# Optimization experiments

Hardware: AMD Instinct MI355X
Metric: run time of the kernel (lower is better)

Reference implementation:

```python
import jax, jax.numpy as jnp
import numpy as np

NUM_GRAPHS = 100  # batch of graphs for pooling (dgl.max_nodes / WeightAndSum)


def _glorot(k, shape):
    lim = np.sqrt(6.0 / (shape[0] + shape[1])).astype(np.float32)
    return jax.random.uniform(k, shape, jnp.float32, -lim, lim)


def setup_inputs() -> dict:
    key = jax.random.key(0)
    ks = jax.random.split(key, 10)
    N, E, D, H = 100000, 1600000, 128, 128
    node_feats = jax.random.normal(ks[0], (N, D), dtype=jnp.float32)
    src = jax.random.randint(ks[1], (E,), 0, N, dtype=jnp.int32)
    dst = jax.random.randint(ks[2], (E,), 0, N, dtype=jnp.int32)
    graph_ids = jnp.sort(jax.random.randint(ks[3], (N,), 0, NUM_GRAPHS, dtype=jnp.int32))
    W1 = _glorot(ks[4], (D, H)); b1 = jnp.zeros((H,), jnp.float32)
    W2 = _glorot(ks[5], (H, H)); b2 = jnp.zeros((H,), jnp.float32)
    W3 = _glorot(ks[6], (H, H)); b3 = jnp.zeros((H,), jnp.float32)
    W_pool = _glorot(ks[7], (H, 1)); b_pool = jnp.zeros((1,), jnp.float32)
    return {"node_feats": node_feats, "src": src, "dst": dst, "graph_ids": graph_ids,
            "W1": W1, "b1": b1, "W2": W2, "b2": b2, "W3": W3, "b3": b3,
            "W_pool": W_pool, "b_pool": b_pool}


def _gcn_layer(h, W, b, src, dst, norm_src, norm_dst, N):
    # DGL GraphConv, norm='both': D_dst^{-1/2} (A^T (D_src^{-1/2} X W)) + b
    h = (h * norm_src[:, None]) @ W                      # [N, H]
    agg = jax.ops.segment_sum(h[src], dst, num_segments=N)  # gather + scatter-add
    return agg * norm_dst[:, None] + b


def reference(node_feats, src, dst, graph_ids, W1, b1, W2, b2, W3, b3, W_pool, b_pool):
    N = node_feats.shape[0]
    # dgl.add_self_loop (allow_zero_in_degree=False)
    loops = jnp.arange(N, dtype=src.dtype)
    src_sl = jnp.concatenate([src, loops])
    dst_sl = jnp.concatenate([dst, loops])
    ones = jnp.ones(src_sl.shape, jnp.float32)
    out_deg = jax.ops.segment_sum(ones, src_sl, num_segments=N)
    in_deg = jax.ops.segment_sum(ones, dst_sl, num_segments=N)
    norm_src = jax.lax.rsqrt(jnp.maximum(out_deg, 1.0))
    norm_dst = jax.lax.rsqrt(jnp.maximum(in_deg, 1.0))
    h = node_feats
    for W, b in ((W1, b1), (W2, b2), (W3, b3)):
        h = jax.nn.relu(_gcn_layer(h, W, b, src_sl, dst_sl, norm_src, norm_dst, N))
    # pooling_func: WeightAndSum (sigmoid-gated weighted sum per graph) + max_nodes
    w = jax.nn.sigmoid(h @ W_pool + b_pool)              # [N, 1]
    g_sum = jax.ops.segment_sum(h * w, graph_ids, num_segments=NUM_GRAPHS)
    g_max = jax.ops.segment_max(h, graph_ids, num_segments=NUM_GRAPHS)
    return jnp.concatenate([g_sum, g_max], axis=1)       # [G, 2H]
```

## Files before the change

kernel.cpp:

```cpp
#include <hip/hip_runtime.h>
#include <hip/hip_bf16.h>

#define DIM 128
#define CAP 64
#define NBMAX 64
#define BCAP 36864
#define CSPLIT 8

typedef __attribute__((ext_vector_type(8))) short bf16x8;
typedef __attribute__((ext_vector_type(4))) float f32x4;
union U16 { uint4 u; bf16x8 b; };

__device__ __forceinline__ unsigned short f2bf(float f) {
    unsigned u = __float_as_uint(f);
    unsigned r = (u + 0x7fffu + ((u >> 16) & 1u)) >> 16;
    return (unsigned short)r;
}
__device__ __forceinline__ unsigned pack2bf(float a, float b) {
    return (unsigned)f2bf(a) | ((unsigned)f2bf(b) << 16);
}
__device__ __forceinline__ float2 unpack2bf(unsigned v) {
    float2 r;
    r.x = __uint_as_float(v << 16);
    r.y = __uint_as_float(v & 0xffff0000u);
    return r;
}
__device__ __forceinline__ void accum8s(float* acc, uint4 v, float s) {
    float2 f0 = unpack2bf(v.x), f1 = unpack2bf(v.y);
    float2 f2 = unpack2bf(v.z), f3 = unpack2bf(v.w);
    acc[0] += s * f0.x; acc[1] += s * f0.y; acc[2] += s * f1.x; acc[3] += s * f1.y;
    acc[4] += s * f2.x; acc[5] += s * f2.y; acc[6] += s * f3.x; acc[7] += s * f3.y;
}

__global__ __launch_bounds__(256) void k_bin(const int* __restrict__ src,
                                             const int* __restrict__ dst, int E,
                                             unsigned* __restrict__ binD,
                                             unsigned short* __restrict__ binS,
                                             int* __restrict__ cntD,
                                             int* __restrict__ cntS, int NB, int binGrid,
                                             const float* __restrict__ W1,
                                             const float* __restrict__ W2,
                                             const float* __restrict__ W3,
                                             unsigned* __restrict__ wT1g,
                                             unsigned* __restrict__ wT2g,
                                             unsigned* __restrict__ wT3g) {
    __shared__ int hD[NBMAX], hS[NBMAX], bD[NBMAX], bS[NBMAX];
    int t = threadIdx.x;
    if ((int)blockIdx.x >= binGrid) {
        int w = blockIdx.x - binGrid;
        const float* Wsrc = (w == 0) ? W1 : (w == 1) ? W2 : W3;
        unsigned* wTg = (w == 0) ? wT1g : (w == 1) ? wT2g : wT3g;
        int n = t >> 1;
        int kp0 = (t & 1) * 32;
#pragma unroll
        for (int i = 0; i < 32; i++) {
            int kp = kp0 + i;
            wTg[n * 64 + kp] = pack2bf(Wsrc[(2 * kp) * DIM + n], Wsrc[(2 * kp + 1) * DIM + n]);
        }
        return;
    }
    if (t < NB) { hD[t] = 0; hS[t] = 0; }
    __syncthreads();
    int e0 = blockIdx.x * 1024 + t * 4;
    int s[4], d[4];
    bool v[4];
#pragma unroll
    for (int i = 0; i < 4; i++) {
        v[i] = (e0 + i) < E;
        s[i] = 0; d[i] = 0;
        if (v[i]) { s[i] = src[e0 + i]; d[i] = dst[e0 + i]; }
    }
#pragma unroll
    for (int i = 0; i < 4; i++) {
        if (v[i]) {
            atomicAdd(&hD[d[i] >> 11], 1);
            atomicAdd(&hS[s[i] >> 11], 1);
        }
    }
    __syncthreads();
    if (t < NB) {
        bD[t] = atomicAdd(&cntD[t], hD[t]);
        bS[t] = atomicAdd(&cntS[t], hS[t]);
        hD[t] = 0; hS[t] = 0;
    }
    __syncthreads();
#pragma unroll
    for (int i = 0; i < 4; i++) {
        if (v[i]) {
            int bd = d[i] >> 11;
            int r = atomicAdd(&hD[bd], 1);
            int idx = bD[bd] + r;
            if (idx < BCAP)
                binD[bd * BCAP + idx] = ((unsigned)(d[i] & 2047) << 17) | (unsigned)s[i];
            int bs = s[i] >> 11;
            int r2 = atomicAdd(&hS[bs], 1);
            int idx2 = bS[bs] + r2;
            if (idx2 < BCAP) binS[bs * BCAP + idx2] = (unsigned short)(s[i] & 2047);
        }
    }
}

__global__ __launch_bounds__(256) void k_mega(const unsigned* __restrict__ binD,
                                              const unsigned short* __restrict__ binS,
                                              const int* __restrict__ cntD,
                                              const int* __restrict__ cntS,
                                              int* __restrict__ in_cnt,
                                              int* __restrict__ out_cnt,
                                              int* __restrict__ csr_pad,
                                              const float* __restrict__ x,
                                              const unsigned* __restrict__ wT1g,
                                              unsigned* __restrict__ xwb, int N,
                                              int NB) {
    __shared__ __align__(16) char smem[34816];
    int bid = blockIdx.x;
    int t = threadIdx.x;

    if (bid < NB * CSPLIT) {
        int b = bid / CSPLIT;
        int sub = bid - b * CSPLIT;
        int* h = (int*)smem;
        int* bArr = ((int*)smem) + 2048;
        for (int j = t; j < 2048; j += 256) h[j] = 0;
        __syncthreads();
        int base = b << 11;
        int nE = cntD[b];
        if (nE > BCAP) nE = BCAP;
        int chunk = (nE + CSPLIT - 1) / CSPLIT;
        int i0 = sub * chunk;
        int i1 = i0 + chunk;
        if (i1 > nE) i1 = nE;
        const unsigned* bb = &binD[b * BCAP];
        for (int i = i0 + t * 4; i < i1; i += 1024) {
            unsigned e[4];
            int k = i1 - i;
            if (k > 4) k = 4;
#pragma unroll
            for (int j = 0; j < 4; j++)
                if (j < k) e[j] = bb[i + j];
#pragma unroll
            for (int j = 0; j < 4; j++)
                if (j < k) atomicAdd(&h[e[j] >> 17], 1);
        }
        __syncthreads();
        for (int j = t; j < 2048; j += 256) {
            int hv = h[j];
            bArr[j] = hv ? atomicAdd(&in_cnt[base + j], hv) : 0;
            h[j] = 0;
        }
        __syncthreads();
        for (int i = i0 + t * 4; i < i1; i += 1024) {
            unsigned e[4];
            int k = i1 - i;
            if (k > 4) k = 4;
#pragma unroll
            for (int j = 0; j < 4; j++)
                if (j < k) e[j] = bb[i + j];
#pragma unroll
            for (int j = 0; j < 4; j++)
                if (j < k) {
                    int dl = (int)(e[j] >> 17);
                    int pos = bArr[dl] + atomicAdd(&h[dl], 1);
                    if (pos < CAP)
                        csr_pad[(size_t)(base + dl) * CAP + pos] = (int)(e[j] & 0x1FFFFu);
                }
        }
        return;
    }
    if (bid < 2 * NB * CSPLIT) {
        int bb2 = bid - NB * CSPLIT;
        int b = bb2 / CSPLIT;
        int sub = bb2 - b * CSPLIT;
        int* hist = (int*)smem;
        for (int j = t; j < 2048; j += 256) hist[j] = 0;
        __syncthreads();
        int base = b << 11;
        int nE = cntS[b];
        if (nE > BCAP) nE = BCAP;
        int chunk = (nE + CSPLIT - 1) / CSPLIT;
        int i0 = sub * chunk;
        int i1 = i0 + chunk;
        if (i1 > nE) i1 = nE;
        const unsigned short* bs = &binS[b * BCAP];
        for (int i = i0 + t * 4; i < i1; i += 1024) {
            unsigned short e[4];
            int k = i1 - i;
            if (k > 4) k = 4;
#pragma unroll
            for (int j = 0; j < 4; j++)
                if (j < k) e[j] = bs[i + j];
#pragma unroll
            for (int j = 0; j < 4; j++)
                if (j < k) atomicAdd(&hist[(int)e[j]], 1);
        }
        __syncthreads();
        for (int j = t; j < 2048; j += 256) {
            int hv = hist[j];
            if (hv) atomicAdd(&out_cnt[base + j], hv);
        }
        return;
    }
    int gb = bid - 2 * NB * CSPLIT;
    unsigned* wT = (unsigned*)smem;
#pragma unroll
    for (int i = 0; i < 8; i++) {
        int idx = t + i * 256;
        int row = idx >> 4;
        int col = idx & 15;
        *(uint4*)&wT[row * 68 + col * 4] = ((const uint4*)wT1g)[idx];
    }
    __syncthreads();
    int wave = t >> 6, lane = t & 63;
    int quad = lane >> 4, c = lane & 15;
    int m = gb * 64 + wave * 16 + c;
    bool mv = m < N;
    f32x4 acc[8];
#pragma unroll
    for (int i = 0; i < 8; i++) acc[i] = (f32x4){0.f, 0.f, 0.f, 0.f};

#pragma unroll
    for (int ks = 0; ks < 4; ks++) {
        U16 av;
        if (mv) {
            const float4* xr = (const float4*)&x[(size_t)m * DIM + ks * 32 + quad * 8];
            float4 f0 = xr[0], f1 = xr[1];
            av.u.x = pack2bf(f0.x, f0.y);
            av.u.y = pack2bf(f0.z, f0.w);
            av.u.z = pack2bf(f1.x, f1.y);
            av.u.w = pack2bf(f1.z, f1.w);
        } else {
            av.u = make_uint4(0, 0, 0, 0);
        }
#pragma unroll
        for (int cb = 0; cb < 8; cb++) {
            U16 bv;
            bv.u = *(const uint4*)&wT[(cb * 16 + c) * 68 + ks * 16 + quad * 4];
            acc[cb] = __builtin_amdgcn_mfma_f32_16x16x32_bf16(av.b, bv.b, acc[cb], 0, 0, 0);
        }
    }
    int rowBase = gb * 64 + wave * 16 + quad * 4;
#pragma unroll
    for (int r = 0; r < 4; r++) {
        int rowN = rowBase + r;
#pragma unroll
        for (int cb = 0; cb < 8; cb++) {
            float v = acc[cb][r];
            float vn = __shfl_xor(v, 1, 64);
            if (((c & 1) == 0) && rowN < N)
                xwb[rowN * 64 + cb * 8 + (c >> 1)] = pack2bf(v, vn);
        }
    }
}

__global__ __launch_bounds__(256) void k_agg1(const uint4* __restrict__ xwb4,
                                              const int* __restrict__ in_cnt,
                                              const int* __restrict__ out_cnt,
                                              const int* __restrict__ csr_pad,
                                              const float* __restrict__ bias,
                                              uint4* __restrict__ hb4, int N) {
    int gid = blockIdx.x * blockDim.x + threadIdx.x;
    int n = gid >> 6;
    int lane = gid & 63;
    if (n >= N) return;
    int quad = lane >> 4;
    int c = lane & 15;

    float acc[8];
#pragma unroll
    for (int i = 0; i < 8; i++) acc[i] = 0.f;

    if (quad == 0) {
        float sn = rsqrtf((float)(out_cnt[n] + 1));
        accum8s(acc, xwb4[n * 16 + c], sn);
    }
    int deg_true = in_cnt[n];
    int deg = deg_true > CAP ? CAP : deg_true;
    const int* row = &csr_pad[(size_t)n * CAP];
    int p = 0;
    for (; p + 16 <= deg; p += 16) {
        int s0 = row[p + quad];
        int s1 = row[p + 4 + quad];
        int s2 = row[p + 8 + quad];
        int s3 = row[p + 12 + quad];
        uint4 v0 = xwb4[s0 * 16 + c];
        uint4 v1 = xwb4[s1 * 16 + c];
        uint4 v2 = xwb4[s2 * 16 + c];
        uint4 v3 = xwb4[s3 * 16 + c];
        float n0 = rsqrtf((float)(out_cnt[s0] + 1));
        float n1 = rsqrtf((float)(out_cnt[s1] + 1));
        float n2 = rsqrtf((float)(out_cnt[s2] + 1));
        float n3 = rsqrtf((float)(out_cnt[s3] + 1));
        accum8s(acc, v0, n0);
        accum8s(acc, v1, n1);
        accum8s(acc, v2, n2);
        accum8s(acc, v3, n3);
    }
    for (; p + 8 <= deg; p += 8) {
        int s0 = row[p + quad];
        int s1 = row[p + 4 + quad];
        uint4 v0 = xwb4[s0 * 16 + c];
        uint4 v1 = xwb4[s1 * 16 + c];
        float n0 = rsqrtf((float)(out_cnt[s0] + 1));
        float n1 = rsqrtf((float)(out_cnt[s1] + 1));
        accum8s(acc, v0, n0);
        accum8s(acc, v1, n1);
    }
    for (; p < deg; p += 4) {
        int pe = p + quad;
        int s = row[pe < deg ? pe : p];
        uint4 v = xwb4[s * 16 + c];
        float ns = rsqrtf((float)(out_cnt[s] + 1));
        if (pe < deg) accum8s(acc, v, ns);
    }
#pragma unroll
    for (int i = 0; i < 8; i++) {
        acc[i] += __shfl_xor(acc[i], 16, 64);
        acc[i] += __shfl_xor(acc[i], 32, 64);
    }
    float ndv = rsqrtf((float)(deg_true + 1));
    if (quad == 0) {
        float4 b0 = ((const float4*)bias)[2 * c];
        float4 b1 = ((const float4*)bias)[2 * c + 1];
        uint4 w;
        w.x = pack2bf(fmaxf(acc[0] * ndv + b0.x, 0.f), fmaxf(acc[1] * ndv + b0.y, 0.f));
        w.y = pack2bf(fmaxf(acc[2] * ndv + b0.z, 0.f), fmaxf(acc[3] * ndv + b0.w, 0.f));
        w.z = pack2bf(fmaxf(acc[4] * ndv + b1.x, 0.f), fmaxf(acc[5] * ndv + b1.y, 0.f));
        w.w = pack2bf(fmaxf(acc[6] * ndv + b1.z, 0.f), fmaxf(acc[7] * ndv + b1.w, 0.f));
        hb4[n * 16 + c] = w;
    }
}

__global__ __launch_bounds__(256) void k_xw_mfma(const unsigned* __restrict__ hb,
                                                 const int* __restrict__ out_cnt,
                                                 const unsigned* __restrict__ wTg,
                                                 unsigned* __restrict__ xwb, int N) {
    __shared__ unsigned wT[128 * 68];
    int t = threadIdx.x;
#pragma unroll
    for (int i = 0; i < 8; i++) {
        int idx = t + i * 256;
        int row = idx >> 4;
        int col = idx & 15;
        *(uint4*)&wT[row * 68 + col * 4] = ((const uint4*)wTg)[idx];
    }
    __syncthreads();
    int wave = t >> 6, lane = t & 63;
    int quad = lane >> 4, c = lane & 15;
    int m = blockIdx.x * 64 + wave * 16 + c;
    bool mv = m < N;
    f32x4 acc[8];
#pragma unroll
    for (int i = 0; i < 8; i++) acc[i] = (f32x4){0.f, 0.f, 0.f, 0.f};

#pragma unroll
    for (int ks = 0; ks < 4; ks++) {
        U16 av;
        if (mv) av.u = *(const uint4*)&hb[m * 64 + ks * 16 + quad * 4];
        else av.u = make_uint4(0, 0, 0, 0);
#pragma unroll
        for (int cb = 0; cb < 8; cb++) {
            U16 bv;
            bv.u = *(const uint4*)&wT[(cb * 16 + c) * 68 + ks * 16 + quad * 4];
            acc[cb] = __builtin_amdgcn_mfma_f32_16x16x32_bf16(av.b, bv.b, acc[cb], 0, 0, 0);
        }
    }
    int rowBase = blockIdx.x * 64 + wave * 16 + quad * 4;
#pragma unroll
    for (int r = 0; r < 4; r++) {
        int rowN = rowBase + r;
        float nrm = (rowN < N) ? rsqrtf((float)(out_cnt[rowN] + 1)) : 0.f;
#pragma unroll
        for (int cb = 0; cb < 8; cb++) {
            float v = acc[cb][r] * nrm;
            float vn = __shfl_xor(v, 1, 64);
            if (((c & 1) == 0) && rowN < N)
                xwb[rowN * 64 + cb * 8 + (c >> 1)] = pack2bf(v, vn);
        }
    }
}

template <bool GATED>
__device__ __forceinline__ void agg_body(const uint4* __restrict__ xwb4,
                                         const int* __restrict__ in_cnt,
                                         const int* __restrict__ csr_pad,
                                         const float* __restrict__ bias,
                                         uint4* __restrict__ hb4,
                                         const float* __restrict__ Wp,
                                         const float* __restrict__ bp,
                                         float* __restrict__ wg, int N) {
    int gid = blockIdx.x * blockDim.x + threadIdx.x;
    int n = gid >> 6;
    int lane = gid & 63;
    if (n >= N) return;
    int quad = lane >> 4;
    int c = lane & 15;

    float acc[8];
#pragma unroll
    for (int i = 0; i < 8; i++) acc[i] = 0.f;

    if (quad == 0) {
        accum8s(acc, xwb4[n * 16 + c], 1.f);
    }
    int deg_true = in_cnt[n];
    int deg = deg_true > CAP ? CAP : deg_true;
    const int* row = &csr_pad[(size_t)n * CAP];
    int p = 0;
    for (; p + 16 <= deg; p += 16) {
        int s0 = row[p + quad];
        int s1 = row[p + 4 + quad];
        int s2 = row[p + 8 + quad];
        int s3 = row[p + 12 + quad];
        uint4 v0 = xwb4[s0 * 16 + c];
        uint4 v1 = xwb4[s1 * 16 + c];
        uint4 v2 = xwb4[s2 * 16 + c];
        uint4 v3 = xwb4[s3 * 16 + c];
        accum8s(acc, v0, 1.f);
        accum8s(acc, v1, 1.f);
        accum8s(acc, v2, 1.f);
        accum8s(acc, v3, 1.f);
    }
    for (; p + 8 <= deg; p += 8) {
        int s0 = row[p + quad];
        int s1 = row[p + 4 + quad];
        uint4 v0 = xwb4[s0 * 16 + c];
        uint4 v1 = xwb4[s1 * 16 + c];
        accum8s(acc, v0, 1.f);
        accum8s(acc, v1, 1.f);
    }
    for (; p < deg; p += 4) {
        int pe = p + quad;
        int s = row[pe < deg ? pe : p];
        uint4 v = xwb4[s * 16 + c];
        if (pe < deg) accum8s(acc, v, 1.f);
    }
#pragma unroll
    for (int i = 0; i < 8; i++) {
        acc[i] += __shfl_xor(acc[i], 16, 64);
        acc[i] += __shfl_xor(acc[i], 32, 64);
    }
    float ndv = rsqrtf((float)(deg_true + 1));
    float4 b0 = ((const float4*)bias)[2 * c];
    float4 b1 = ((const float4*)bias)[2 * c + 1];
    float o[8];
    o[0] = fmaxf(acc[0] * ndv + b0.x, 0.f);
    o[1] = fmaxf(acc[1] * ndv + b0.y, 0.f);
    o[2] = fmaxf(acc[2] * ndv + b0.z, 0.f);
    o[3] = fmaxf(acc[3] * ndv + b0.w, 0.f);
    o[4] = fmaxf(acc[4] * ndv + b1.x, 0.f);
    o[5] = fmaxf(acc[5] * ndv + b1.y, 0.f);
    o[6] = fmaxf(acc[6] * ndv + b1.z, 0.f);
    o[7] = fmaxf(acc[7] * ndv + b1.w, 0.f);
    if (quad == 0) {
        uint4 w;
        w.x = pack2bf(o[0], o[1]);
        w.y = pack2bf(o[2], o[3]);
        w.z = pack2bf(o[4], o[5]);
        w.w = pack2bf(o[6], o[7]);
        hb4[n * 16 + c] = w;
    }
    if (GATED) {
        float s = 0.f;
        if (quad == 0) {
            float4 w0 = ((const float4*)Wp)[2 * c];
            float4 w1 = ((const float4*)Wp)[2 * c + 1];
            s = o[0] * w0.x + o[1] * w0.y + o[2] * w0.z + o[3] * w0.w +
                o[4] * w1.x + o[5] * w1.y + o[6] * w1.z + o[7] * w1.w;
        }
        s += __shfl_xor(s, 1, 64);
        s += __shfl_xor(s, 2, 64);
        s += __shfl_xor(s, 4, 64);
        s += __shfl_xor(s, 8, 64);
        if (lane == 0) wg[n] = 1.f / (1.f + expf(-(s + bp[0])));
    }
}

__global__ __launch_bounds__(256) void k_agg(const uint4* __restrict__ xwb4,
                                             const int* __restrict__ in_cnt,
                                             const int* __restrict__ csr_pad,
                                             const float* __restrict__ bias,
                                             uint4* __restrict__ hb4, int N) {
    agg_body<false>(xwb4, in_cnt, csr_pad, bias, hb4, nullptr, nullptr, nullptr, N);
}

__global__ __launch_bounds__(256) void k_agg_gate(const uint4* __restrict__ xwb4,
                                                  const int* __restrict__ in_cnt,
                                                  const int* __restrict__ csr_pad,
                                                  const float* __restrict__ bias,
                                                  uint4* __restrict__ hb4,
                                                  const float* __restrict__ Wp,
                                                  const float* __restrict__ bp,
                                                  float* __restrict__ wg, int N) {
    agg_body<true>(xwb4, in_cnt, csr_pad, bias, hb4, Wp, bp, wg, N);
}

__device__ __forceinline__ int lower_bound(const int* a, int n, int key) {
    int lo = 0, hi = n;
    while (lo < hi) {
        int m = (lo + hi) >> 1;
        if (a[m] < key) lo = m + 1;
        else hi = m;
    }
    return lo;
}

__global__ __launch_bounds__(64) void k_pool(const unsigned* __restrict__ hb,
                                             const float* __restrict__ wg,
                                             const int* __restrict__ gids,
                                             float* __restrict__ out, int N) {
    int g = blockIdx.x >> 4;
    int part = blockIdx.x & 15;
    int t = threadIdx.x;
    int start = lower_bound(gids, N, g);
    int end = lower_bound(gids, N, g + 1);
    float2 sum = {0.f, 0.f}, mx = {0.f, 0.f};
    for (int n = start + part; n < end; n += 16) {
        float w = wg[n];
        float2 v = unpack2bf(hb[n * 64 + t]);
        sum.x += v.x * w;
        sum.y += v.y * w;
        mx.x = fmaxf(mx.x, v.x);
        mx.y = fmaxf(mx.y, v.y);
    }
    atomicAdd(&out[g * 256 + 2 * t], sum.x);
    atomicAdd(&out[g * 256 + 2 * t + 1], sum.y);
    atomicMax((int*)&out[g * 256 + 128 + 2 * t], __float_as_int(mx.x));
    atomicMax((int*)&out[g * 256 + 128 + 2 * t + 1], __float_as_int(mx.y));
}

extern "C" void kernel_launch(void* const* d_in, const int* in_sizes, int n_in,
                              void* d_out, int out_size, void* d_ws, size_t ws_size,
                              hipStream_t stream) {
    const float* node_feats = (const float*)d_in[0];
    const int* src = (const int*)d_in[1];
    const int* dst = (const int*)d_in[2];
    const int* gids = (const int*)d_in[3];
    const float* W1 = (const float*)d_in[4];
    const float* b1 = (const float*)d_in[5];
    const float* W2 = (const float*)d_in[6];
    const float* b2 = (const float*)d_in[7];
    const float* W3 = (const float*)d_in[8];
    const float* b3 = (const float*)d_in[9];
    const float* Wp = (const float*)d_in[10];
    const float* bp = (const float*)d_in[11];
    float* out = (float*)d_out;

    const int N = in_sizes[3];
    const int E = in_sizes[1];
    const int G = out_size / 256;
    const int NB = (N + 2047) >> 11;

    char* ws = (char*)d_ws;
    size_t o = 0;
    int* cntD = (int*)(ws + o);          o += NBMAX * 4;
    int* cntS = (int*)(ws + o);          o += NBMAX * 4;
    int* in_cnt = (int*)(ws + o);        o += (size_t)N * 4;
    int* out_cnt = (int*)(ws + o);       o += (size_t)N * 4;
    size_t zero_bytes = o;
    float* wg = (float*)(ws + o);        o += (size_t)N * 4;
    o = (o + 15) & ~15ull;
    unsigned* wT1g = (unsigned*)(ws + o); o += 8192 * 4;
    unsigned* wT2g = (unsigned*)(ws + o); o += 8192 * 4;
    unsigned* wT3g = (unsigned*)(ws + o); o += 8192 * 4;
    unsigned* binD = (unsigned*)(ws + o); o += (size_t)NBMAX * BCAP * 4;
    unsigned short* binS = (unsigned short*)(ws + o); o += (size_t)NBMAX * BCAP * 2;
    o = (o + 15) & ~15ull;
    int* csr_pad = (int*)(ws + o);       o += (size_t)N * CAP * 4;
    unsigned* xwb = (unsigned*)(ws + o); o += (size_t)N * 64 * 4;
    unsigned* hb = (unsigned*)(ws + o);  o += (size_t)N * 64 * 4;
    (void)ws_size;

    (void)hipMemsetAsync(d_ws, 0, zero_bytes, stream);
    (void)hipMemsetAsync(d_out, 0, (size_t)out_size * 4, stream);

    int binGrid = (E + 1023) / 1024;
    int mmGrid = (N + 63) / 64;
    int aggGrid = ((N * 64) + 255) / 256;

    k_bin<<<binGrid + 3, 256, 0, stream>>>(src, dst, E, binD, binS, cntD, cntS, NB, binGrid,
                                           W1, W2, W3, wT1g, wT2g, wT3g);
    k_mega<<<2 * NB * CSPLIT + mmGrid, 256, 0, stream>>>(binD, binS, cntD, cntS, in_cnt,
                                                         out_cnt, csr_pad, node_feats,
                                                         wT1g, xwb, N, NB);
    k_agg1<<<aggGrid, 256, 0, stream>>>((const uint4*)xwb, in_cnt, out_cnt, csr_pad, b1,
                                        (uint4*)hb, N);
    k_xw_mfma<<<mmGrid, 256, 0, stream>>>(hb, out_cnt, wT2g, xwb, N);
    k_agg<<<aggGrid, 256, 0, stream>>>((const uint4*)xwb, in_cnt, csr_pad, b2,
                                       (uint4*)hb, N);
    k_xw_mfma<<<mmGrid, 256, 0, stream>>>(hb, out_cnt, wT3g, xwb, N);
    k_agg_gate<<<aggGrid, 256, 0, stream>>>((const uint4*)xwb, in_cnt, csr_pad, b3,
                                            (uint4*)hb, Wp, bp, wg, N);
    k_pool<<<G * 16, 64, 0, stream>>>(hb, wg, gids, out, N);
}
```

Baseline: 454.4 us.

## Map four nodes per wave in aggregation kernels and precompute source norms

The aggregation kernels now give each 16-lane group of a wave its own destination node and walk that node's edges serially, four at a time. Previously the four quads split one node's edges and then merged results with cross-quad shuffles. This removes the shuffle reduction, lets every lane do useful epilogue work and store, and launches a quarter as many threads. A new small kernel precomputes the per-node source-norm rsqrt once, so layer 1 no longer recomputes it for every edge, and accumulation uses fma with native bf16 conversion. The risk is divergence between the four nodes of a wave when their degrees differ, and slightly different memory-level parallelism per node.

```diff
diff --git a/kernel.cpp b/kernel.cpp
--- a/kernel.cpp
+++ b/kernel.cpp
@@ -9,7 +9,9 @@
 
 typedef __attribute__((ext_vector_type(8))) short bf16x8;
 typedef __attribute__((ext_vector_type(4))) float f32x4;
+typedef __bf16 bf16x2 __attribute__((ext_vector_type(2)));
 union U16 { uint4 u; bf16x8 b; };
+union UB { unsigned u; bf16x2 h; };
 
 __device__ __forceinline__ unsigned short f2bf(float f) {
     unsigned u = __float_as_uint(f);
@@ -30,6 +32,18 @@
     float2 f2 = unpack2bf(v.z), f3 = unpack2bf(v.w);
     acc[0] += s * f0.x; acc[1] += s * f0.y; acc[2] += s * f1.x; acc[3] += s * f1.y;
     acc[4] += s * f2.x; acc[5] += s * f2.y; acc[6] += s * f3.x; acc[7] += s * f3.y;
+}
+__device__ __forceinline__ void accum8m(float* acc, uint4 v, float s) {
+    UB w0, w1, w2, w3;
+    w0.u = v.x; w1.u = v.y; w2.u = v.z; w3.u = v.w;
+    acc[0] = fmaf((float)w0.h[0], s, acc[0]);
+    acc[1] = fmaf((float)w0.h[1], s, acc[1]);
+    acc[2] = fmaf((float)w1.h[0], s, acc[2]);
+    acc[3] = fmaf((float)w1.h[1], s, acc[3]);
+    acc[4] = fmaf((float)w2.h[0], s, acc[4]);
+    acc[5] = fmaf((float)w2.h[1], s, acc[5]);
+    acc[6] = fmaf((float)w3.h[0], s, acc[6]);
+    acc[7] = fmaf((float)w3.h[1], s, acc[7]);
 }
 
 __global__ __launch_bounds__(256) void k_bin(const int* __restrict__ src,
@@ -251,227 +265,109 @@
     }
 }
 
-__global__ __launch_bounds__(256) void k_agg1(const uint4* __restrict__ xwb4,
-                                              const int* __restrict__ in_cnt,
-                                              const int* __restrict__ out_cnt,
-                                              const int* __restrict__ csr_pad,
-                                              const float* __restrict__ bias,
-                                              uint4* __restrict__ hb4, int N) {
-    int gid = blockIdx.x * blockDim.x + threadIdx.x;
-    int n = gid >> 6;
-    int lane = gid & 63;
-    if (n >= N) return;
-    int quad = lane >> 4;
-    int c = lane & 15;
-
-    float acc[8];
-#pragma unroll
-    for (int i = 0; i < 8; i++) acc[i] = 0.f;
-
-    if (quad == 0) {
-        float sn = rsqrtf((float)(out_cnt[n] + 1));
-        accum8s(acc, xwb4[n * 16 + c], sn);
-    }
-    int deg_true = in_cnt[n];
-    int deg = deg_true > CAP ? CAP : deg_true;
-    const int* row = &csr_pad[(size_t)n * CAP];
-    int p = 0;
-    for (; p + 16 <= deg; p += 16) {
-        int s0 = row[p + quad];
-        int s1 = row[p + 4 + quad];
-        int s2 = row[p + 8 + quad];
-        int s3 = row[p + 12 + quad];
-        uint4 v0 = xwb4[s0 * 16 + c];
-        uint4 v1 = xwb4[s1 * 16 + c];
-        uint4 v2 = xwb4[s2 * 16 + c];
-        uint4 v3 = xwb4[s3 * 16 + c];
-        float n0 = rsqrtf((float)(out_cnt[s0] + 1));
-        float n1 = rsqrtf((float)(out_cnt[s1] + 1));
-        float n2 = rsqrtf((float)(out_cnt[s2] + 1));
-        float n3 = rsqrtf((float)(out_cnt[s3] + 1));
-        accum8s(acc, v0, n0);
-        accum8s(acc, v1, n1);
-        accum8s(acc, v2, n2);
-        accum8s(acc, v3, n3);
-    }
-    for (; p + 8 <= deg; p += 8) {
-        int s0 = row[p + quad];
-        int s1 = row[p + 4 + quad];
-        uint4 v0 = xwb4[s0 * 16 + c];
-        uint4 v1 = xwb4[s1 * 16 + c];
-        float n0 = rsqrtf((float)(out_cnt[s0] + 1));
-        float n1 = rsqrtf((float)(out_cnt[s1] + 1));
-        accum8s(acc, v0, n0);
-        accum8s(acc, v1, n1);
-    }
-    for (; p < deg; p += 4) {
-        int pe = p + quad;
-        int s = row[pe < deg ? pe : p];
-        uint4 v = xwb4[s * 16 + c];
-        float ns = rsqrtf((float)(out_cnt[s] + 1));
-        if (pe < deg) accum8s(acc, v, ns);
-    }
-#pragma unroll
-    for (int i = 0; i < 8; i++) {
-        acc[i] += __shfl_xor(acc[i], 16, 64);
-        acc[i] += __shfl_xor(acc[i], 32, 64);
-    }
-    float ndv = rsqrtf((float)(deg_true + 1));
-    if (quad == 0) {
-        float4 b0 = ((const float4*)bias)[2 * c];
-        float4 b1 = ((const float4*)bias)[2 * c + 1];
-        uint4 w;
-        w.x = pack2bf(fmaxf(acc[0] * ndv + b0.x, 0.f), fmaxf(acc[1] * ndv + b0.y, 0.f));
-        w.y = pack2bf(fmaxf(acc[2] * ndv + b0.z, 0.f), fmaxf(acc[3] * ndv + b0.w, 0.f));
-        w.z = pack2bf(fmaxf(acc[4] * ndv + b1.x, 0.f), fmaxf(acc[5] * ndv + b1.y, 0.f));
-        w.w = pack2bf(fmaxf(acc[6] * ndv + b1.z, 0.f), fmaxf(acc[7] * ndv + b1.w, 0.f));
-        hb4[n * 16 + c] = w;
-    }
-}
-
-__global__ __launch_bounds__(256) void k_xw_mfma(const unsigned* __restrict__ hb,
-                                                 const int* __restrict__ out_cnt,
-                                                 const unsigned* __restrict__ wTg,
-                                                 unsigned* __restrict__ xwb, int N) {
-    __shared__ unsigned wT[128 * 68];
-    int t = threadIdx.x;
-#pragma unroll
-    for (int i = 0; i < 8; i++) {
-        int idx = t + i * 256;
-        int row = idx >> 4;
-        int col = idx & 15;
-        *(uint4*)&wT[row * 68 + col * 4] = ((const uint4*)wTg)[idx];
-    }
-    __syncthreads();
-    int wave = t >> 6, lane = t & 63;
-    int quad = lane >> 4, c = lane & 15;
-    int m = blockIdx.x * 64 + wave * 16 + c;
-    bool mv = m < N;
-    f32x4 acc[8];
-#pragma unroll
-    for (int i = 0; i < 8; i++) acc[i] = (f32x4){0.f, 0.f, 0.f, 0.f};
-
-#pragma unroll
-    for (int ks = 0; ks < 4; ks++) {
-        U16 av;
-        if (mv) av.u = *(const uint4*)&hb[m * 64 + ks * 16 + quad * 4];
-        else av.u = make_uint4(0, 0, 0, 0);
-#pragma unroll
-        for (int cb = 0; cb < 8; cb++) {
-            U16 bv;
-            bv.u = *(const uint4*)&wT[(cb * 16 + c) * 68 + ks * 16 + quad * 4];
-            acc[cb] = __builtin_amdgcn_mfma_f32_16x16x32_bf16(av.b, bv.b, acc[cb], 0, 0, 0);
-        }
-    }
-    int rowBase = blockIdx.x * 64 + wave * 16 + quad * 4;
-#pragma unroll
-    for (int r = 0; r < 4; r++) {
-        int rowN = rowBase + r;
-        float nrm = (rowN < N) ? rsqrtf((float)(out_cnt[rowN] + 1)) : 0.f;
-#pragma unroll
-        for (int cb = 0; cb < 8; cb++) {
-            float v = acc[cb][r] * nrm;
-            float vn = __shfl_xor(v, 1, 64);
-            if (((c & 1) == 0) && rowN < N)
-                xwb[rowN * 64 + cb * 8 + (c >> 1)] = pack2bf(v, vn);
-        }
-    }
-}
-
-template <bool GATED>
+__global__ __launch_bounds__(256) void k_nrm(const int* __restrict__ out_cnt,
+                                             float* __restrict__ nsv, int N) {
+    int i = (blockIdx.x * 256 + threadIdx.x) * 4;
+    if (i + 3 < N) {
+        int4 d = *(const int4*)&out_cnt[i];
+        float4 r;
+        r.x = rsqrtf((float)(d.x + 1));
+        r.y = rsqrtf((float)(d.y + 1));
+        r.z = rsqrtf((float)(d.z + 1));
+        r.w = rsqrtf((float)(d.w + 1));
+        *(float4*)&nsv[i] = r;
+    } else {
+        for (int j = i; j < N && j < i + 4; j++) nsv[j] = rsqrtf((float)(out_cnt[j] + 1));
+    }
+}
+
+template <int MODE>
 __device__ __forceinline__ void agg_body(const uint4* __restrict__ xwb4,
                                          const int* __restrict__ in_cnt,
                                          const int* __restrict__ csr_pad,
+                                         const float* __restrict__ nsv,
                                          const float* __restrict__ bias,
                                          uint4* __restrict__ hb4,
                                          const float* __restrict__ Wp,
                                          const float* __restrict__ bp,
                                          float* __restrict__ wg, int N) {
-    int gid = blockIdx.x * blockDim.x + threadIdx.x;
-    int n = gid >> 6;
-    int lane = gid & 63;
-    if (n >= N) return;
-    int quad = lane >> 4;
-    int c = lane & 15;
+    int wid = (blockIdx.x * 256 + threadIdx.x) >> 6;
+    int lane = threadIdx.x & 63;
+    int g = lane >> 4, c = lane & 15;
+    int n = wid * 4 + g;
+    bool nv = n < N;
+    int deg_true = nv ? in_cnt[n] : 0;
+    int deg = deg_true > CAP ? CAP : deg_true;
+    float ndv = rsqrtf((float)(deg_true + 1));
+    const int* row = csr_pad + (size_t)n * CAP;
 
     float acc[8];
 #pragma unroll
     for (int i = 0; i < 8; i++) acc[i] = 0.f;
 
-    if (quad == 0) {
-        accum8s(acc, xwb4[n * 16 + c], 1.f);
-    }
-    int deg_true = in_cnt[n];
-    int deg = deg_true > CAP ? CAP : deg_true;
-    const int* row = &csr_pad[(size_t)n * CAP];
-    int p = 0;
-    for (; p + 16 <= deg; p += 16) {
-        int s0 = row[p + quad];
-        int s1 = row[p + 4 + quad];
-        int s2 = row[p + 8 + quad];
-        int s3 = row[p + 12 + quad];
-        uint4 v0 = xwb4[s0 * 16 + c];
-        uint4 v1 = xwb4[s1 * 16 + c];
-        uint4 v2 = xwb4[s2 * 16 + c];
-        uint4 v3 = xwb4[s3 * 16 + c];
-        accum8s(acc, v0, 1.f);
-        accum8s(acc, v1, 1.f);
-        accum8s(acc, v2, 1.f);
-        accum8s(acc, v3, 1.f);
-    }
-    for (; p + 8 <= deg; p += 8) {
-        int s0 = row[p + quad];
-        int s1 = row[p + 4 + quad];
-        uint4 v0 = xwb4[s0 * 16 + c];
-        uint4 v1 = xwb4[s1 * 16 + c];
-        accum8s(acc, v0, 1.f);
-        accum8s(acc, v1, 1.f);
-    }
-    for (; p < deg; p += 4) {
-        int pe = p + quad;
-        int s = row[pe < deg ? pe : p];
-        uint4 v = xwb4[s * 16 + c];
-        if (pe < deg) accum8s(acc, v, 1.f);
-    }
-#pragma unroll
-    for (int i = 0; i < 8; i++) {
-        acc[i] += __shfl_xor(acc[i], 16, 64);
-        acc[i] += __shfl_xor(acc[i], 32, 64);
-    }
-    float ndv = rsqrtf((float)(deg_true + 1));
+    if (nv) {
+        float s0 = (MODE == 0) ? nsv[n] : ndv;
+        accum8m(acc, xwb4[(size_t)n * 16 + c], s0);
+    }
+    for (int p = 0; p < deg; p += 4) {
+        int sidx[4];
+        uint4 gv[4];
+        float sc[4];
+        bool pv[4];
+#pragma unroll
+        for (int u = 0; u < 4; u++) {
+            pv[u] = (p + u) < deg;
+            sidx[u] = pv[u] ? row[p + u] : row[p];
+        }
+#pragma unroll
+        for (int u = 0; u < 4; u++) gv[u] = xwb4[(size_t)sidx[u] * 16 + c];
+#pragma unroll
+        for (int u = 0; u < 4; u++) sc[u] = (MODE == 0) ? nsv[sidx[u]] : ndv;
+#pragma unroll
+        for (int u = 0; u < 4; u++)
+            if (pv[u]) accum8m(acc, gv[u], sc[u]);
+    }
+
+    float mul = (MODE == 0) ? ndv : 1.f;
     float4 b0 = ((const float4*)bias)[2 * c];
     float4 b1 = ((const float4*)bias)[2 * c + 1];
     float o[8];
-    o[0] = fmaxf(acc[0] * ndv + b0.x, 0.f);
-    o[1] = fmaxf(acc[1] * ndv + b0.y, 0.f);
-    o[2] = fmaxf(acc[2] * ndv + b0.z, 0.f);
-    o[3] = fmaxf(acc[3] * ndv + b0.w, 0.f);
-    o[4] = fmaxf(acc[4] * ndv + b1.x, 0.f);
-    o[5] = fmaxf(acc[5] * ndv + b1.y, 0.f);
-    o[6] = fmaxf(acc[6] * ndv + b1.z, 0.f);
-    o[7] = fmaxf(acc[7] * ndv + b1.w, 0.f);
-    if (quad == 0) {
+    o[0] = fmaxf(acc[0] * mul + b0.x, 0.f);
+    o[1] = fmaxf(acc[1] * mul + b0.y, 0.f);
+    o[2] = fmaxf(acc[2] * mul + b0.z, 0.f);
+    o[3] = fmaxf(acc[3] * mul + b0.w, 0.f);
+    o[4] = fmaxf(acc[4] * mul + b1.x, 0.f);
+    o[5] = fmaxf(acc[5] * mul + b1.y, 0.f);
+    o[6] = fmaxf(acc[6] * mul + b1.z, 0.f);
+    o[7] = fmaxf(acc[7] * mul + b1.w, 0.f);
+    if (nv) {
         uint4 w;
         w.x = pack2bf(o[0], o[1]);
         w.y = pack2bf(o[2], o[3]);
         w.z = pack2bf(o[4], o[5]);
         w.w = pack2bf(o[6], o[7]);
-        hb4[n * 16 + c] = w;
-    }
-    if (GATED) {
-        float s = 0.f;
-        if (quad == 0) {
-            float4 w0 = ((const float4*)Wp)[2 * c];
-            float4 w1 = ((const float4*)Wp)[2 * c + 1];
-            s = o[0] * w0.x + o[1] * w0.y + o[2] * w0.z + o[3] * w0.w +
-                o[4] * w1.x + o[5] * w1.y + o[6] * w1.z + o[7] * w1.w;
-        }
+        hb4[(size_t)n * 16 + c] = w;
+    }
+    if (MODE == 2) {
+        float4 w0 = ((const float4*)Wp)[2 * c];
+        float4 w1 = ((const float4*)Wp)[2 * c + 1];
+        float s = o[0] * w0.x + o[1] * w0.y + o[2] * w0.z + o[3] * w0.w +
+                  o[4] * w1.x + o[5] * w1.y + o[6] * w1.z + o[7] * w1.w;
         s += __shfl_xor(s, 1, 64);
         s += __shfl_xor(s, 2, 64);
         s += __shfl_xor(s, 4, 64);
         s += __shfl_xor(s, 8, 64);
-        if (lane == 0) wg[n] = 1.f / (1.f + expf(-(s + bp[0])));
-    }
+        if (nv && c == 0) wg[n] = 1.f / (1.f + expf(-(s + bp[0])));
+    }
+}
+
+__global__ __launch_bounds__(256) void k_agg1(const uint4* __restrict__ xwb4,
+                                              const int* __restrict__ in_cnt,
+                                              const int* __restrict__ csr_pad,
+                                              const float* __restrict__ nsv,
+                                              const float* __restrict__ bias,
+                                              uint4* __restrict__ hb4, int N) {
+    agg_body<0>(xwb4, in_cnt, csr_pad, nsv, bias, hb4, nullptr, nullptr, nullptr, N);
 }
 
 __global__ __launch_bounds__(256) void k_agg(const uint4* __restrict__ xwb4,
@@ -479,7 +375,7 @@
                                              const int* __restrict__ csr_pad,
                                              const float* __restrict__ bias,
                                              uint4* __restrict__ hb4, int N) {
-    agg_body<false>(xwb4, in_cnt, csr_pad, bias, hb4, nullptr, nullptr, nullptr, N);
+    agg_body<1>(xwb4, in_cnt, csr_pad, nullptr, bias, hb4, nullptr, nullptr, nullptr, N);
 }
 
 __global__ __launch_bounds__(256) void k_agg_gate(const uint4* __restrict__ xwb4,
@@ -490,7 +386,56 @@
                                                   const float* __restrict__ Wp,
                                                   const float* __restrict__ bp,
                                                   float* __restrict__ wg, int N) {
-    agg_body<true>(xwb4, in_cnt, csr_pad, bias, hb4, Wp, bp, wg, N);
+    agg_body<2>(xwb4, in_cnt, csr_pad, nullptr, bias, hb4, Wp, bp, wg, N);
+}
+
+__global__ __launch_bounds__(256) void k_xw_mfma(const unsigned* __restrict__ hb,
+                                                 const int* __restrict__ out_cnt,
+                                                 const unsigned* __restrict__ wTg,
+                                                 unsigned* __restrict__ xwb, int N) {
+    __shared__ unsigned wT[128 * 68];
+    int t = threadIdx.x;
+#pragma unroll
+    for (int i = 0; i < 8; i++) {
+        int idx = t + i * 256;
+        int row = idx >> 4;
+        int col = idx & 15;
+        *(uint4*)&wT[row * 68 + col * 4] = ((const uint4*)wTg)[idx];
+    }
+    __syncthreads();
+    int wave = t >> 6, lane = t & 63;
+    int quad = lane >> 4, c = lane & 15;
+    int m = blockIdx.x * 64 + wave * 16 + c;
+    bool mv = m < N;
+    f32x4 acc[8];
+#pragma unroll
+    for (int i = 0; i < 8; i++) acc[i] = (f32x4){0.f, 0.f, 0.f, 0.f};
+
+#pragma unroll
+    for (int ks = 0; ks < 4; ks++) {
+        U16 av;
+        if (mv) av.u = *(const uint4*)&hb[m * 64 + ks * 16 + quad * 4];
+        else av.u = make_uint4(0, 0, 0, 0);
+#pragma unroll
+        for (int cb = 0; cb < 8; cb++) {
+            U16 bv;
+            bv.u = *(const uint4*)&wT[(cb * 16 + c) * 68 + ks * 16 + quad * 4];
+            acc[cb] = __builtin_amdgcn_mfma_f32_16x16x32_bf16(av.b, bv.b, acc[cb], 0, 0, 0);
+        }
+    }
+    int rowBase = blockIdx.x * 64 + wave * 16 + quad * 4;
+#pragma unroll
+    for (int r = 0; r < 4; r++) {
+        int rowN = rowBase + r;
+        float nrm = (rowN < N) ? rsqrtf((float)(out_cnt[rowN] + 1)) : 0.f;
+#pragma unroll
+        for (int cb = 0; cb < 8; cb++) {
+            float v = acc[cb][r] * nrm;
+            float vn = __shfl_xor(v, 1, 64);
+            if (((c & 1) == 0) && rowN < N)
+                xwb[rowN * 64 + cb * 8 + (c >> 1)] = pack2bf(v, vn);
+        }
+    }
 }
 
 __device__ __forceinline__ int lower_bound(const int* a, int n, int key) {
@@ -557,6 +502,7 @@
     int* out_cnt = (int*)(ws + o);       o += (size_t)N * 4;
     size_t zero_bytes = o;
     float* wg = (float*)(ws + o);        o += (size_t)N * 4;
+    float* nsv = (float*)(ws + o);       o += (size_t)N * 4;
     o = (o + 15) & ~15ull;
     unsigned* wT1g = (unsigned*)(ws + o); o += 8192 * 4;
     unsigned* wT2g = (unsigned*)(ws + o); o += 8192 * 4;
@@ -574,14 +520,16 @@
 
     int binGrid = (E + 1023) / 1024;
     int mmGrid = (N + 63) / 64;
-    int aggGrid = ((N * 64) + 255) / 256;
+    int aggGrid = (N + 15) / 16;
+    int nrmGrid = (N + 1023) / 1024;
 
     k_bin<<<binGrid + 3, 256, 0, stream>>>(src, dst, E, binD, binS, cntD, cntS, NB, binGrid,
                                            W1, W2, W3, wT1g, wT2g, wT3g);
     k_mega<<<2 * NB * CSPLIT + mmGrid, 256, 0, stream>>>(binD, binS, cntD, cntS, in_cnt,
                                                          out_cnt, csr_pad, node_feats,
                                                          wT1g, xwb, N, NB);
-    k_agg1<<<aggGrid, 256, 0, stream>>>((const uint4*)xwb, in_cnt, out_cnt, csr_pad, b1,
+    k_nrm<<<nrmGrid, 256, 0, stream>>>(out_cnt, nsv, N);
+    k_agg1<<<aggGrid, 256, 0, stream>>>((const uint4*)xwb, in_cnt, csr_pad, nsv, b1,
                                         (uint4*)hb, N);
     k_xw_mfma<<<mmGrid, 256, 0, stream>>>(hb, out_cnt, wT2g, xwb, N);
     k_agg<<<aggGrid, 256, 0, stream>>>((const uint4*)xwb, in_cnt, csr_pad, b2,
```

Result: no change. 456.4 us (+0.4%).
